# Kernel tuning notes

Hardware: AMD Instinct MI355X
Metric: run time of the kernel (lower is better)

## Reference

```python
import jax, jax.numpy as jnp
import numpy as np

B, S = 64, 32
VF, IF = 512, 256
F = VF + IF        # fused feature dim == sensory dim
U = 768            # wiring units == rnn_hidden_dim (motor_size == units)
UNFOLDS = 6        # ncps LTC default ode_unfolds
EPS = 1e-8


def setup_inputs() -> dict:
    key = jax.random.key(0)
    ks = jax.random.split(key, 24)
    d = {}
    d['fv'] = jax.random.normal(ks[0], (B, S, VF), jnp.float32)
    d['fv_alter'] = jax.random.normal(ks[1], (B, S, VF), jnp.float32)
    d['fi'] = jax.random.normal(ks[2], (B, S, IF), jnp.float32)
    d['dec'] = jax.random.normal(ks[3], (B, S, 2), jnp.float32)
    # strictly increasing timestamps so relative timespans are positive
    d['ts'] = jnp.cumsum(jax.random.uniform(ks[4], (B, S + 1), jnp.float32, 0.01, 0.1), axis=1)
    # LTC cell parameters (ncps init ranges), FullyConnected wiring -> dense masks of ones
    d['input_w'] = jnp.ones((F,), jnp.float32)
    d['input_b'] = jnp.zeros((F,), jnp.float32)
    d['sensory_mu'] = jax.random.uniform(ks[5], (F, U), jnp.float32, 0.3, 0.8)
    d['sensory_sigma'] = jax.random.uniform(ks[6], (F, U), jnp.float32, 3.0, 8.0)
    d['sensory_w'] = jax.random.uniform(ks[7], (F, U), jnp.float32, 0.001, 1.0)
    d['sensory_erev'] = jnp.sign(jax.random.normal(ks[8], (F, U), jnp.float32))
    d['mu'] = jax.random.uniform(ks[9], (U, U), jnp.float32, 0.3, 0.8)
    d['sigma'] = jax.random.uniform(ks[10], (U, U), jnp.float32, 3.0, 8.0)
    d['w'] = jax.random.uniform(ks[11], (U, U), jnp.float32, 0.001, 1.0)
    d['erev'] = jnp.sign(jax.random.normal(ks[12], (U, U), jnp.float32))
    d['gleak'] = jax.random.uniform(ks[13], (U,), jnp.float32, 0.001, 1.0)
    d['vleak'] = jax.random.uniform(ks[14], (U,), jnp.float32, -0.2, 0.2)
    d['cm'] = jax.random.uniform(ks[15], (U,), jnp.float32, 0.4, 0.6)
    d['output_w'] = jnp.ones((U,), jnp.float32)
    d['output_b'] = jnp.zeros((U,), jnp.float32)
    d['W1'] = jax.random.normal(ks[16], (U, 128), jnp.float32) / np.sqrt(U)
    d['b1'] = jnp.zeros((128,), jnp.float32)
    d['W2'] = jax.random.normal(ks[17], (128, 6), jnp.float32) / np.sqrt(128.0)
    d['b2'] = jnp.zeros((6,), jnp.float32)
    return d


def _ltc(fused, rel_ts, input_w, input_b, sensory_mu, sensory_sigma, sensory_w,
         sensory_erev, mu, sigma, w, erev, gleak, vleak, cm, output_w, output_b):
    b = fused.shape[0]
    h0 = jnp.zeros((b, U), fused.dtype)

    def step(v, xs):
        inp, elapsed = xs  # (B,F), (B,)
        x = inp * input_w + input_b
        # sensory synapse activations: (B, F, U)
        s_act = sensory_w * jax.nn.sigmoid(sensory_sigma * (x[:, :, None] - sensory_mu))
        w_num_s = jnp.einsum('bfu,fu->bu', s_act, sensory_erev)
        w_den_s = jnp.sum(s_act, axis=1)
        cm_t = cm / (elapsed[:, None] / UNFOLDS)  # (B,U)

        def unfold(vv, _):
            act = w * jax.nn.sigmoid(sigma * (vv[:, :, None] - mu))  # (B,U,U)
            num = jnp.einsum('buv,uv->bv', act, erev) + w_num_s
            den = jnp.sum(act, axis=1) + w_den_s
            vv = (cm_t * vv + gleak * vleak + num) / (cm_t + gleak + den + EPS)
            return vv, None

        v, _ = jax.lax.scan(unfold, v, None, length=UNFOLDS)
        out = v * output_w + output_b  # motor_size == units
        return v, out

    _, outs = jax.lax.scan(step, h0, (jnp.swapaxes(fused, 0, 1), rel_ts.T))
    return jnp.swapaxes(outs, 0, 1), h0  # (B,S,U)


def reference(fv, fv_alter, fi, dec, ts, input_w, input_b, sensory_mu, sensory_sigma,
              sensory_w, sensory_erev, mu, sigma, w, erev, gleak, vleak, cm,
              output_w, output_b, W1, b1, W2, b2):
    fused = jnp.concatenate([fv, fi], axis=-1)  # FusionModule 'cat'
    rel_ts = ts[:, 1:] - ts[:, :-1]
    h_seq, h0 = _ltc(fused, rel_ts, input_w, input_b, sensory_mu, sensory_sigma,
                     sensory_w, sensory_erev, mu, sigma, w, erev, gleak, vleak, cm,
                     output_w, output_b)
    x = (h_seq - h0[:, None, :]) @ W1 + b1
    x = jnp.where(x > 0, x, 0.1 * x)  # LeakyReLU(0.1)
    pose = x @ W2 + b2
    return pose[:, None], h_seq  # (B,1,S,6), (B,S,U)
```

## Files before the change

kernel.cpp:

```cpp
#include <hip/hip_runtime.h>

#define Bq 64
#define Sq 32
#define VFq 512
#define IFq 256
#define Fq 768
#define Uq 768
#define UNFq 6
#define L2E 1.44269504088896340736f
typedef unsigned long long ull;

template <int CTRL>
__device__ __forceinline__ float dpp_add(float x) {
  int t = __builtin_amdgcn_update_dpp(0, __builtin_bit_cast(int, x), CTRL, 0xF, 0xF, true);
  return x + __builtin_bit_cast(float, t);
}
__device__ __forceinline__ float swz_add4(float x) {
  int t = __builtin_amdgcn_ds_swizzle(__builtin_bit_cast(int, x), 0x101F);
  return x + __builtin_bit_cast(float, t);
}

__global__ __launch_bounds__(256) void k_prep(
    const float* __restrict__ smu, const float* __restrict__ ssig,
    const float* __restrict__ sw,  const float* __restrict__ ser,
    const float* __restrict__ rmu, const float* __restrict__ rsig,
    const float* __restrict__ rw,  const float* __restrict__ rer,
    const float* __restrict__ ts,
    float4* __restrict__ Ps, float4* __restrict__ Pr,
    float* __restrict__ iel, unsigned* __restrict__ flags)
{
  int bid = blockIdx.x, tid = threadIdx.x;
  if (bid < 1152) {
    int set = bid / 576, tile = bid % 576;
    int tv = tile / 24, tu = tile % 24;
    const float* Amu = set ? rmu : smu;
    const float* Asg = set ? rsig : ssig;
    const float* Aw  = set ? rw  : sw;
    const float* Aer = set ? rer : ser;
    float4* P = set ? Pr : Ps;
    __shared__ float4 tl[32][33];
    int cu = tid & 31, r0 = tid >> 5;
    for (int rr = 0; rr < 32; rr += 8) {
      int v = tv*32 + r0 + rr, u = tu*32 + cu;
      int idx = v*Uq + u;
      float sg = Asg[idx], m = Amu[idx], ww = Aw[idx], er = Aer[idx];
      tl[cu][r0+rr] = make_float4(-sg*L2E, sg*m*L2E, ww, ww*er);
    }
    __syncthreads();
    for (int rr = 0; rr < 32; rr += 8) {
      int u = tu*32 + r0 + rr, v = tv*32 + (tid & 31);
      P[u*Fq + v] = tl[r0+rr][tid & 31];
    }
  } else {
    for (int i = tid; i < Bq*Sq; i += 256) {
      int b = i / Sq, t = i % Sq;
      iel[i] = (float)UNFq / (ts[b*(Sq+1)+t+1] - ts[b*(Sq+1)+t]);
    }
    for (int i = tid; i < 1024; i += 256) flags[i] = 0u;
  }
}

__global__ __launch_bounds__(768) void k_sensory(
    const float* __restrict__ fv, const float* __restrict__ fi,
    const float* __restrict__ iw, const float* __restrict__ ib,
    const float4* __restrict__ Ps,
    float* __restrict__ wns, float* __restrict__ wds)
{
  __shared__ float xs[16][Fq];
  __shared__ float scr[12][8][33];
  int tid = threadIdx.x;
  int bt_tile = blockIdx.x >> 6;
  int ut = blockIdx.x & 63;
  int u0 = ut * 12, bt0 = bt_tile * 16;
  {
    float wv = iw[tid], bv = ib[tid];
    for (int j = 0; j < 16; ++j) {
      int bt = bt0 + j, b = bt >> 5, t = bt & 31;
      float raw = (tid < VFq) ? fv[(b*Sq + t)*VFq + tid]
                              : fi[(b*Sq + t)*IFq + (tid - VFq)];
      xs[j][tid] = raw * wv + bv;
    }
  }
  __syncthreads();
  int w = tid >> 6, l = tid & 63;
  const float4* P = Ps + (u0 + w)*Fq;
  #pragma unroll
  for (int pass = 0; pass < 4; ++pass) {
    float num[4], den[4];
    #pragma unroll
    for (int q = 0; q < 4; ++q) { num[q] = 0.f; den[q] = 0.f; }
    for (int i = 0; i < 12; ++i) {
      int f = l + 64*i;
      float4 p = P[f];
      #pragma unroll
      for (int q = 0; q < 4; ++q) {
        float arg = fmaf(p.x, xs[4*pass + q][f], p.y);
        float e = __builtin_amdgcn_exp2f(arg);
        float r = __builtin_amdgcn_rcpf(1.0f + e);
        den[q] = fmaf(p.z, r, den[q]);
        num[q] = fmaf(p.w, r, num[q]);
      }
    }
    #pragma unroll
    for (int q = 0; q < 4; ++q) {
      num[q] = dpp_add<0xB1>(num[q]); den[q] = dpp_add<0xB1>(den[q]);
      num[q] = dpp_add<0x4E>(num[q]); den[q] = dpp_add<0x4E>(den[q]);
      num[q] = swz_add4(num[q]);      den[q] = swz_add4(den[q]);
    }
    if ((l & 7) == 0) {
      int rep = l >> 3;
      #pragma unroll
      for (int q = 0; q < 4; ++q) {
        scr[w][rep][4*pass + q] = num[q];
        scr[w][rep][16 + 4*pass + q] = den[q];
      }
    }
    __builtin_amdgcn_sched_barrier(0);
  }
  __syncthreads();
  if (tid < 192) {
    int u = tid >> 4, j = tid & 15;
    float nt = 0.f, dt = 0.f;
    #pragma unroll
    for (int rep = 0; rep < 8; ++rep) { nt += scr[u][rep][j]; dt += scr[u][rep][16+j]; }
    int bt = bt0 + j, b = bt >> 5, t = bt & 31;
    wns[(t*Bq + b)*Uq + (u0 + u)] = nt;
    wds[(t*Bq + b)*Uq + (u0 + u)] = dt;
  }
}

__global__ __launch_bounds__(768)
void k_recurrent(
    const float4* __restrict__ Pr,
    const float* __restrict__ wns, const float* __restrict__ wds,
    float* __restrict__ vg, const float* __restrict__ iel,
    unsigned* __restrict__ flags,
    const float* __restrict__ gleak, const float* __restrict__ vleak,
    const float* __restrict__ cm, const float* __restrict__ ow,
    const float* __restrict__ ob, float* __restrict__ hout)
{
  __shared__ float4 vvP[4][Uq];
  __shared__ float2 scr2[12][8][9];
  __shared__ float sinv[16][Sq];
  __shared__ float swn[2][96], swd[2][96];
  __shared__ float sgl[12], sglvl[12], scm[12], sow[12], sob[12];
  int tid = threadIdx.x;
  int g = blockIdx.x >> 6;
  int ut = blockIdx.x & 63;
  int u0 = ut*12, b0 = g*16;
  if (tid < 512) { int j = tid >> 5, t = tid & 31; sinv[j][t] = iel[(b0+j)*Sq + t]; }
  if (tid < 12) {
    float gl0 = gleak[u0+tid];
    sgl[tid] = gl0; sglvl[tid] = gl0 * vleak[u0+tid];
    scm[tid] = cm[u0+tid]; sow[tid] = ow[u0+tid]; sob[tid] = ob[u0+tid];
  }
  #pragma unroll
  for (int q = 0; q < 4; ++q) vvP[q][tid] = make_float4(0.f, 0.f, 0.f, 0.f);
  int w = tid >> 6, l = tid & 63;
  float4 Prg[12];
  #pragma unroll
  for (int i = 0; i < 12; ++i) Prg[i] = Pr[(u0 + w)*Uq + l + 64*i];
  __syncthreads();
  int uu8 = tid >> 3, jv = tid & 7;
  for (int t = 0; t < Sq; ++t) {
    if (tid < 96) {
      swn[0][tid] = wns[(t*Bq + b0 + jv)*Uq + u0 + uu8];
      swd[0][tid] = wds[(t*Bq + b0 + jv)*Uq + u0 + uu8];
      swn[1][tid] = wns[(t*Bq + b0 + 8 + jv)*Uq + u0 + uu8];
      swd[1][tid] = wds[(t*Bq + b0 + 8 + jv)*Uq + u0 + uu8];
    }
    for (int k = 0; k < UNFq; ++k) {
      int p = t*UNFq + k;
      #pragma unroll
      for (int h = 0; h < 2; ++h) {
        int hp = 1 - h;
        float num0[4], den0[4], num1[4], den1[4];
        #pragma unroll
        for (int q = 0; q < 4; ++q) { num0[q] = 0.f; den0[q] = 0.f; }
        #pragma unroll
        for (int i = 0; i < 12; ++i) {
          int v = l + 64*i;
          float4 pp = Prg[i];
          float4 y = vvP[2*h][v];
          float r0 = __builtin_amdgcn_rcpf(1.0f + __builtin_amdgcn_exp2f(fmaf(pp.x, y.x, pp.y)));
          float r1 = __builtin_amdgcn_rcpf(1.0f + __builtin_amdgcn_exp2f(fmaf(pp.x, y.y, pp.y)));
          float r2 = __builtin_amdgcn_rcpf(1.0f + __builtin_amdgcn_exp2f(fmaf(pp.x, y.z, pp.y)));
          float r3 = __builtin_amdgcn_rcpf(1.0f + __builtin_amdgcn_exp2f(fmaf(pp.x, y.w, pp.y)));
          den0[0] = fmaf(pp.z, r0, den0[0]); num0[0] = fmaf(pp.w, r0, num0[0]);
          den0[1] = fmaf(pp.z, r1, den0[1]); num0[1] = fmaf(pp.w, r1, num0[1]);
          den0[2] = fmaf(pp.z, r2, den0[2]); num0[2] = fmaf(pp.w, r2, num0[2]);
          den0[3] = fmaf(pp.z, r3, den0[3]); num0[3] = fmaf(pp.w, r3, num0[3]);
        }
        #pragma unroll
        for (int q = 0; q < 4; ++q) {
          num0[q] = dpp_add<0xB1>(num0[q]); den0[q] = dpp_add<0xB1>(den0[q]);
          num0[q] = dpp_add<0x4E>(num0[q]); den0[q] = dpp_add<0x4E>(den0[q]);
          num0[q] = swz_add4(num0[q]);      den0[q] = swz_add4(den0[q]);
        }
        if ((l & 7) == 0) {
          int r = l >> 3;
          #pragma unroll
          for (int q = 0; q < 4; ++q) scr2[w][r][q] = make_float2(num0[q], den0[q]);
        }
        __builtin_amdgcn_sched_barrier(0);
        ull ga0 = 0, ga1 = 0, ga2 = 0, ga3 = 0;
        bool do_g = !(p == 0 && h == 0);
        if (do_g) {
          const unsigned* f = flags + hp*256 + g*64 + l;
          unsigned tgt = (unsigned)(p + h);
          while (true) {
            unsigned vf = __hip_atomic_load(f, __ATOMIC_RELAXED, __HIP_MEMORY_SCOPE_AGENT);
            if (__ballot(vf < tgt) == 0ull) break;
            __builtin_amdgcn_s_sleep(1);
          }
          const ull* src = (const ull*)(vg + (hp*4 + g)*Uq*8) + tid*4;
          ga0 = __hip_atomic_load(src + 0, __ATOMIC_RELAXED, __HIP_MEMORY_SCOPE_AGENT);
          ga1 = __hip_atomic_load(src + 1, __ATOMIC_RELAXED, __HIP_MEMORY_SCOPE_AGENT);
          ga2 = __hip_atomic_load(src + 2, __ATOMIC_RELAXED, __HIP_MEMORY_SCOPE_AGENT);
          ga3 = __hip_atomic_load(src + 3, __ATOMIC_RELAXED, __HIP_MEMORY_SCOPE_AGENT);
        }
        __builtin_amdgcn_sched_barrier(0);
        #pragma unroll
        for (int q = 0; q < 4; ++q) { num1[q] = 0.f; den1[q] = 0.f; }
        #pragma unroll
        for (int i = 0; i < 12; ++i) {
          int v = l + 64*i;
          float4 pp = Prg[i];
          float4 y = vvP[2*h+1][v];
          float r0 = __builtin_amdgcn_rcpf(1.0f + __builtin_amdgcn_exp2f(fmaf(pp.x, y.x, pp.y)));
          float r1 = __builtin_amdgcn_rcpf(1.0f + __builtin_amdgcn_exp2f(fmaf(pp.x, y.y, pp.y)));
          float r2 = __builtin_amdgcn_rcpf(1.0f + __builtin_amdgcn_exp2f(fmaf(pp.x, y.z, pp.y)));
          float r3 = __builtin_amdgcn_rcpf(1.0f + __builtin_amdgcn_exp2f(fmaf(pp.x, y.w, pp.y)));
          den1[0] = fmaf(pp.z, r0, den1[0]); num1[0] = fmaf(pp.w, r0, num1[0]);
          den1[1] = fmaf(pp.z, r1, den1[1]); num1[1] = fmaf(pp.w, r1, num1[1]);
          den1[2] = fmaf(pp.z, r2, den1[2]); num1[2] = fmaf(pp.w, r2, num1[2]);
          den1[3] = fmaf(pp.z, r3, den1[3]); num1[3] = fmaf(pp.w, r3, num1[3]);
        }
        #pragma unroll
        for (int q = 0; q < 4; ++q) {
          num1[q] = dpp_add<0xB1>(num1[q]); den1[q] = dpp_add<0xB1>(den1[q]);
          num1[q] = dpp_add<0x4E>(num1[q]); den1[q] = dpp_add<0x4E>(den1[q]);
          num1[q] = swz_add4(num1[q]);      den1[q] = swz_add4(den1[q]);
        }
        if ((l & 7) == 0) {
          int r = l >> 3;
          #pragma unroll
          for (int q = 0; q < 4; ++q) scr2[w][r][4+q] = make_float2(num1[q], den1[q]);
        }
        if (do_g) {
          float2 t0 = __builtin_bit_cast(float2, ga0);
          float2 t1 = __builtin_bit_cast(float2, ga1);
          float2 t2 = __builtin_bit_cast(float2, ga2);
          float2 t3 = __builtin_bit_cast(float2, ga3);
          vvP[2*hp+0][tid] = make_float4(t0.x, t0.y, t1.x, t1.y);
          vvP[2*hp+1][tid] = make_float4(t2.x, t2.y, t3.x, t3.y);
        }
        __syncthreads();
        if (tid < 96) {
          float nt = swn[h][tid], dt = swd[h][tid];
          #pragma unroll
          for (int r = 0; r < 8; ++r) { float2 s = scr2[uu8][r][jv]; nt += s.x; dt += s.y; }
          int jh = h*8 + jv;
          float cmt = scm[uu8] * sinv[jh][t];
          const float* vrow = (const float*)&vvP[2*h + (jv >> 2)][u0 + uu8];
          float vold = vrow[jv & 3];
          float vnew = (cmt*vold + sglvl[uu8] + nt)
                     * __builtin_amdgcn_rcpf(cmt + sgl[uu8] + dt + 1e-8f);
          __hip_atomic_store(&vg[(h*4 + g)*Uq*8 + (u0 + uu8)*8 + jv], vnew,
                             __ATOMIC_RELAXED, __HIP_MEMORY_SCOPE_AGENT);
          if (k == UNFq-1)
            hout[((b0 + jh)*Sq + t)*Uq + u0 + uu8] = fmaf(vnew, sow[uu8], sob[uu8]);
        }
        __builtin_amdgcn_s_waitcnt(0);
        __syncthreads();
        if (tid == 0)
          __hip_atomic_store(&flags[h*256 + g*64 + ut], (unsigned)(p + 1),
                             __ATOMIC_RELAXED, __HIP_MEMORY_SCOPE_AGENT);
      }
    }
  }
}

__global__ __launch_bounds__(128) void k_head(
    const float* __restrict__ hseq, const float* __restrict__ W1,
    const float* __restrict__ b1, const float* __restrict__ W2,
    const float* __restrict__ b2, float* __restrict__ pose)
{
  __shared__ float h[Uq];
  __shared__ float x1[128];
  int bt = blockIdx.x, tid = threadIdx.x;
  for (int j = 0; j < 6; ++j) h[tid + 128*j] = hseq[bt*Uq + tid + 128*j];
  __syncthreads();
  float acc = b1[tid];
  for (int f = 0; f < Uq; ++f) acc = fmaf(h[f], W1[f*128 + tid], acc);
  x1[tid] = acc > 0.f ? acc : 0.1f*acc;
  __syncthreads();
  if (tid < 6) {
    float a2 = b2[tid];
    #pragma unroll
    for (int c = 0; c < 128; ++c) a2 = fmaf(x1[c], W2[c*6 + tid], a2);
    pose[bt*6 + tid] = a2;
  }
}

extern "C" void kernel_launch(void* const* d_in, const int* in_sizes, int n_in,
                              void* d_out, int out_size, void* d_ws, size_t ws_size,
                              hipStream_t stream) {
  const float* fv   = (const float*)d_in[0];
  const float* fi   = (const float*)d_in[2];
  const float* ts   = (const float*)d_in[4];
  const float* iw   = (const float*)d_in[5];
  const float* ibb  = (const float*)d_in[6];
  const float* smu  = (const float*)d_in[7];
  const float* ssig = (const float*)d_in[8];
  const float* sw   = (const float*)d_in[9];
  const float* ser  = (const float*)d_in[10];
  const float* rmu  = (const float*)d_in[11];
  const float* rsig = (const float*)d_in[12];
  const float* rw   = (const float*)d_in[13];
  const float* rer  = (const float*)d_in[14];
  const float* gl   = (const float*)d_in[15];
  const float* vl   = (const float*)d_in[16];
  const float* cm   = (const float*)d_in[17];
  const float* ow   = (const float*)d_in[18];
  const float* ob   = (const float*)d_in[19];
  const float* W1   = (const float*)d_in[20];
  const float* b1   = (const float*)d_in[21];
  const float* W2   = (const float*)d_in[22];
  const float* b2   = (const float*)d_in[23];

  float* pose = (float*)d_out;
  float* hseq = (float*)d_out + Bq*Sq*6;

  float* ws = (float*)d_ws;
  float4* Ps = (float4*)ws;
  float4* Pr = (float4*)(ws + 2359296);
  float* wns = ws + 4718592;
  float* wds = ws + 6291456;
  float* vg  = ws + 7864320;
  float* iel = ws + 7962624;
  unsigned* flags = (unsigned*)(ws + 7964672);

  k_prep<<<1153, 256, 0, stream>>>(smu, ssig, sw, ser, rmu, rsig, rw, rer,
                                   ts, Ps, Pr, iel, flags);
  k_sensory<<<8192, 768, 0, stream>>>(fv, fi, iw, ibb, Ps, wns, wds);
  k_recurrent<<<256, 768, 0, stream>>>(Pr, wns, wds, vg, iel, flags,
                                       gl, vl, cm, ow, ob, hseq);
  k_head<<<2048, 128, 0, stream>>>(hseq, W1, b1, W2, b2, pose);
}
```

Before: 2.425 ms.

## Finalize recurrent update per wave with swizzle reductions and packed FMAs

```diff
diff --git a/kernel.cpp b/kernel.cpp
--- a/kernel.cpp
+++ b/kernel.cpp
@@ -9,14 +9,16 @@
 #define UNFq 6
 #define L2E 1.44269504088896340736f
 typedef unsigned long long ull;
+typedef __attribute__((ext_vector_type(2))) float f2;
 
 template <int CTRL>
 __device__ __forceinline__ float dpp_add(float x) {
   int t = __builtin_amdgcn_update_dpp(0, __builtin_bit_cast(int, x), CTRL, 0xF, 0xF, true);
   return x + __builtin_bit_cast(float, t);
 }
-__device__ __forceinline__ float swz_add4(float x) {
-  int t = __builtin_amdgcn_ds_swizzle(__builtin_bit_cast(int, x), 0x101F);
+template <int OFF>
+__device__ __forceinline__ float swz_add(float x) {
+  int t = __builtin_amdgcn_ds_swizzle(__builtin_bit_cast(int, x), OFF);
   return x + __builtin_bit_cast(float, t);
 }
 
@@ -86,33 +88,31 @@
   const float4* P = Ps + (u0 + w)*Fq;
   #pragma unroll
   for (int pass = 0; pass < 4; ++pass) {
-    float num[4], den[4];
+    f2 acc[4];
     #pragma unroll
-    for (int q = 0; q < 4; ++q) { num[q] = 0.f; den[q] = 0.f; }
+    for (int q = 0; q < 4; ++q) acc[q] = (f2){0.f, 0.f};
     for (int i = 0; i < 12; ++i) {
       int f = l + 64*i;
       float4 p = P[f];
+      f2 pwz = (f2){p.w, p.z};
       #pragma unroll
       for (int q = 0; q < 4; ++q) {
         float arg = fmaf(p.x, xs[4*pass + q][f], p.y);
         float e = __builtin_amdgcn_exp2f(arg);
         float r = __builtin_amdgcn_rcpf(1.0f + e);
-        den[q] = fmaf(p.z, r, den[q]);
-        num[q] = fmaf(p.w, r, num[q]);
+        acc[q] = __builtin_elementwise_fma(pwz, (f2){r, r}, acc[q]);
       }
     }
     #pragma unroll
     for (int q = 0; q < 4; ++q) {
-      num[q] = dpp_add<0xB1>(num[q]); den[q] = dpp_add<0xB1>(den[q]);
-      num[q] = dpp_add<0x4E>(num[q]); den[q] = dpp_add<0x4E>(den[q]);
-      num[q] = swz_add4(num[q]);      den[q] = swz_add4(den[q]);
-    }
-    if ((l & 7) == 0) {
-      int rep = l >> 3;
-      #pragma unroll
-      for (int q = 0; q < 4; ++q) {
-        scr[w][rep][4*pass + q] = num[q];
-        scr[w][rep][16 + 4*pass + q] = den[q];
+      float num = acc[q].x, den = acc[q].y;
+      num = dpp_add<0xB1>(num); den = dpp_add<0xB1>(den);
+      num = dpp_add<0x4E>(num); den = dpp_add<0x4E>(den);
+      num = swz_add<0x101F>(num); den = swz_add<0x101F>(den);
+      if ((l & 7) == 0) {
+        int rep = l >> 3;
+        scr[w][rep][4*pass + q] = num;
+        scr[w][rep][16 + 4*pass + q] = den;
       }
     }
     __builtin_amdgcn_sched_barrier(0);
@@ -142,65 +142,61 @@
   __shared__ float4 vvP[4][Uq];
   __shared__ float2 scr2[12][8][9];
   __shared__ float sinv[16][Sq];
-  __shared__ float swn[2][96], swd[2][96];
-  __shared__ float sgl[12], sglvl[12], scm[12], sow[12], sob[12];
   int tid = threadIdx.x;
   int g = blockIdx.x >> 6;
   int ut = blockIdx.x & 63;
   int u0 = ut*12, b0 = g*16;
   if (tid < 512) { int j = tid >> 5, t = tid & 31; sinv[j][t] = iel[(b0+j)*Sq + t]; }
-  if (tid < 12) {
-    float gl0 = gleak[u0+tid];
-    sgl[tid] = gl0; sglvl[tid] = gl0 * vleak[u0+tid];
-    scm[tid] = cm[u0+tid]; sow[tid] = ow[u0+tid]; sob[tid] = ob[u0+tid];
-  }
   #pragma unroll
   for (int q = 0; q < 4; ++q) vvP[q][tid] = make_float4(0.f, 0.f, 0.f, 0.f);
   int w = tid >> 6, l = tid & 63;
+  float my_gl   = gleak[u0 + w];
+  float my_glvl = my_gl * vleak[u0 + w];
+  float my_cm   = cm[u0 + w];
+  float my_ow   = ow[u0 + w];
+  float my_ob   = ob[u0 + w];
   float4 Prg[12];
   #pragma unroll
   for (int i = 0; i < 12; ++i) Prg[i] = Pr[(u0 + w)*Uq + l + 64*i];
   __syncthreads();
-  int uu8 = tid >> 3, jv = tid & 7;
+  int jl = l & 7;
   for (int t = 0; t < Sq; ++t) {
-    if (tid < 96) {
-      swn[0][tid] = wns[(t*Bq + b0 + jv)*Uq + u0 + uu8];
-      swd[0][tid] = wds[(t*Bq + b0 + jv)*Uq + u0 + uu8];
-      swn[1][tid] = wns[(t*Bq + b0 + 8 + jv)*Uq + u0 + uu8];
-      swd[1][tid] = wds[(t*Bq + b0 + 8 + jv)*Uq + u0 + uu8];
-    }
+    float wn0 = wns[(t*Bq + b0 + jl)*Uq + u0 + w];
+    float wd0 = wds[(t*Bq + b0 + jl)*Uq + u0 + w];
+    float wn1 = wns[(t*Bq + b0 + 8 + jl)*Uq + u0 + w];
+    float wd1 = wds[(t*Bq + b0 + 8 + jl)*Uq + u0 + w];
     for (int k = 0; k < UNFq; ++k) {
       int p = t*UNFq + k;
       #pragma unroll
       for (int h = 0; h < 2; ++h) {
         int hp = 1 - h;
-        float num0[4], den0[4], num1[4], den1[4];
-        #pragma unroll
-        for (int q = 0; q < 4; ++q) { num0[q] = 0.f; den0[q] = 0.f; }
-        #pragma unroll
-        for (int i = 0; i < 12; ++i) {
-          int v = l + 64*i;
-          float4 pp = Prg[i];
-          float4 y = vvP[2*h][v];
-          float r0 = __builtin_amdgcn_rcpf(1.0f + __builtin_amdgcn_exp2f(fmaf(pp.x, y.x, pp.y)));
-          float r1 = __builtin_amdgcn_rcpf(1.0f + __builtin_amdgcn_exp2f(fmaf(pp.x, y.y, pp.y)));
-          float r2 = __builtin_amdgcn_rcpf(1.0f + __builtin_amdgcn_exp2f(fmaf(pp.x, y.z, pp.y)));
-          float r3 = __builtin_amdgcn_rcpf(1.0f + __builtin_amdgcn_exp2f(fmaf(pp.x, y.w, pp.y)));
-          den0[0] = fmaf(pp.z, r0, den0[0]); num0[0] = fmaf(pp.w, r0, num0[0]);
-          den0[1] = fmaf(pp.z, r1, den0[1]); num0[1] = fmaf(pp.w, r1, num0[1]);
-          den0[2] = fmaf(pp.z, r2, den0[2]); num0[2] = fmaf(pp.w, r2, num0[2]);
-          den0[3] = fmaf(pp.z, r3, den0[3]); num0[3] = fmaf(pp.w, r3, num0[3]);
-        }
-        #pragma unroll
-        for (int q = 0; q < 4; ++q) {
-          num0[q] = dpp_add<0xB1>(num0[q]); den0[q] = dpp_add<0xB1>(den0[q]);
-          num0[q] = dpp_add<0x4E>(num0[q]); den0[q] = dpp_add<0x4E>(den0[q]);
-          num0[q] = swz_add4(num0[q]);      den0[q] = swz_add4(den0[q]);
-        }
-        if ((l & 7) == 0) {
-          int r = l >> 3;
-          #pragma unroll
-          for (int q = 0; q < 4; ++q) scr2[w][r][q] = make_float2(num0[q], den0[q]);
+        {
+          f2 acc[4];
+          #pragma unroll
+          for (int q = 0; q < 4; ++q) acc[q] = (f2){0.f, 0.f};
+          #pragma unroll
+          for (int i = 0; i < 12; ++i) {
+            int v = l + 64*i;
+            float4 pp = Prg[i];
+            f2 pwz = (f2){pp.w, pp.z};
+            float4 y = vvP[2*h][v];
+            float r0 = __builtin_amdgcn_rcpf(1.0f + __builtin_amdgcn_exp2f(fmaf(pp.x, y.x, pp.y)));
+            float r1 = __builtin_amdgcn_rcpf(1.0f + __builtin_amdgcn_exp2f(fmaf(pp.x, y.y, pp.y)));
+            float r2 = __builtin_amdgcn_rcpf(1.0f + __builtin_amdgcn_exp2f(fmaf(pp.x, y.z, pp.y)));
+            float r3 = __builtin_amdgcn_rcpf(1.0f + __builtin_amdgcn_exp2f(fmaf(pp.x, y.w, pp.y)));
+            acc[0] = __builtin_elementwise_fma(pwz, (f2){r0, r0}, acc[0]);
+            acc[1] = __builtin_elementwise_fma(pwz, (f2){r1, r1}, acc[1]);
+            acc[2] = __builtin_elementwise_fma(pwz, (f2){r2, r2}, acc[2]);
+            acc[3] = __builtin_elementwise_fma(pwz, (f2){r3, r3}, acc[3]);
+          }
+          #pragma unroll
+          for (int q = 0; q < 4; ++q) {
+            float num = acc[q].x, den = acc[q].y;
+            num = dpp_add<0xB1>(num); den = dpp_add<0xB1>(den);
+            num = dpp_add<0x4E>(num); den = dpp_add<0x4E>(den);
+            num = swz_add<0x101F>(num); den = swz_add<0x101F>(den);
+            if ((l & 7) == 0) scr2[w][l >> 3][q] = make_float2(num, den);
+          }
         }
         __builtin_amdgcn_sched_barrier(0);
         ull ga0 = 0, ga1 = 0, ga2 = 0, ga3 = 0;
@@ -220,32 +216,33 @@
           ga3 = __hip_atomic_load(src + 3, __ATOMIC_RELAXED, __HIP_MEMORY_SCOPE_AGENT);
         }
         __builtin_amdgcn_sched_barrier(0);
-        #pragma unroll
-        for (int q = 0; q < 4; ++q) { num1[q] = 0.f; den1[q] = 0.f; }
-        #pragma unroll
-        for (int i = 0; i < 12; ++i) {
-          int v = l + 64*i;
-          float4 pp = Prg[i];
-          float4 y = vvP[2*h+1][v];
-          float r0 = __builtin_amdgcn_rcpf(1.0f + __builtin_amdgcn_exp2f(fmaf(pp.x, y.x, pp.y)));
-          float r1 = __builtin_amdgcn_rcpf(1.0f + __builtin_amdgcn_exp2f(fmaf(pp.x, y.y, pp.y)));
-          float r2 = __builtin_amdgcn_rcpf(1.0f + __builtin_amdgcn_exp2f(fmaf(pp.x, y.z, pp.y)));
-          float r3 = __builtin_amdgcn_rcpf(1.0f + __builtin_amdgcn_exp2f(fmaf(pp.x, y.w, pp.y)));
-          den1[0] = fmaf(pp.z, r0, den1[0]); num1[0] = fmaf(pp.w, r0, num1[0]);
-          den1[1] = fmaf(pp.z, r1, den1[1]); num1[1] = fmaf(pp.w, r1, num1[1]);
-          den1[2] = fmaf(pp.z, r2, den1[2]); num1[2] = fmaf(pp.w, r2, num1[2]);
-          den1[3] = fmaf(pp.z, r3, den1[3]); num1[3] = fmaf(pp.w, r3, num1[3]);
-        }
-        #pragma unroll
-        for (int q = 0; q < 4; ++q) {
-          num1[q] = dpp_add<0xB1>(num1[q]); den1[q] = dpp_add<0xB1>(den1[q]);
-          num1[q] = dpp_add<0x4E>(num1[q]); den1[q] = dpp_add<0x4E>(den1[q]);
-          num1[q] = swz_add4(num1[q]);      den1[q] = swz_add4(den1[q]);
-        }
-        if ((l & 7) == 0) {
-          int r = l >> 3;
-          #pragma unroll
-          for (int q = 0; q < 4; ++q) scr2[w][r][4+q] = make_float2(num1[q], den1[q]);
+        {
+          f2 acc[4];
+          #pragma unroll
+          for (int q = 0; q < 4; ++q) acc[q] = (f2){0.f, 0.f};
+          #pragma unroll
+          for (int i = 0; i < 12; ++i) {
+            int v = l + 64*i;
+            float4 pp = Prg[i];
+            f2 pwz = (f2){pp.w, pp.z};
+            float4 y = vvP[2*h+1][v];
+            float r0 = __builtin_amdgcn_rcpf(1.0f + __builtin_amdgcn_exp2f(fmaf(pp.x, y.x, pp.y)));
+            float r1 = __builtin_amdgcn_rcpf(1.0f + __builtin_amdgcn_exp2f(fmaf(pp.x, y.y, pp.y)));
+            float r2 = __builtin_amdgcn_rcpf(1.0f + __builtin_amdgcn_exp2f(fmaf(pp.x, y.z, pp.y)));
+            float r3 = __builtin_amdgcn_rcpf(1.0f + __builtin_amdgcn_exp2f(fmaf(pp.x, y.w, pp.y)));
+            acc[0] = __builtin_elementwise_fma(pwz, (f2){r0, r0}, acc[0]);
+            acc[1] = __builtin_elementwise_fma(pwz, (f2){r1, r1}, acc[1]);
+            acc[2] = __builtin_elementwise_fma(pwz, (f2){r2, r2}, acc[2]);
+            acc[3] = __builtin_elementwise_fma(pwz, (f2){r3, r3}, acc[3]);
+          }
+          #pragma unroll
+          for (int q = 0; q < 4; ++q) {
+            float num = acc[q].x, den = acc[q].y;
+            num = dpp_add<0xB1>(num); den = dpp_add<0xB1>(den);
+            num = dpp_add<0x4E>(num); den = dpp_add<0x4E>(den);
+            num = swz_add<0x101F>(num); den = swz_add<0x101F>(den);
+            if ((l & 7) == 0) scr2[w][l >> 3][4 + q] = make_float2(num, den);
+          }
         }
         if (do_g) {
           float2 t0 = __builtin_bit_cast(float2, ga0);
@@ -255,21 +252,25 @@
           vvP[2*hp+0][tid] = make_float4(t0.x, t0.y, t1.x, t1.y);
           vvP[2*hp+1][tid] = make_float4(t2.x, t2.y, t3.x, t3.y);
         }
-        __syncthreads();
-        if (tid < 96) {
-          float nt = swn[h][tid], dt = swd[h][tid];
-          #pragma unroll
-          for (int r = 0; r < 8; ++r) { float2 s = scr2[uu8][r][jv]; nt += s.x; dt += s.y; }
-          int jh = h*8 + jv;
-          float cmt = scm[uu8] * sinv[jh][t];
-          const float* vrow = (const float*)&vvP[2*h + (jv >> 2)][u0 + uu8];
-          float vold = vrow[jv & 3];
-          float vnew = (cmt*vold + sglvl[uu8] + nt)
-                     * __builtin_amdgcn_rcpf(cmt + sgl[uu8] + dt + 1e-8f);
-          __hip_atomic_store(&vg[(h*4 + g)*Uq*8 + (u0 + uu8)*8 + jv], vnew,
-                             __ATOMIC_RELAXED, __HIP_MEMORY_SCOPE_AGENT);
-          if (k == UNFq-1)
-            hout[((b0 + jh)*Sq + t)*Uq + u0 + uu8] = fmaf(vnew, sow[uu8], sob[uu8]);
+        {
+          float2 me = scr2[w][l >> 3][jl];
+          float nn = me.x, dd = me.y;
+          nn = swz_add<0x201F>(nn); dd = swz_add<0x201F>(dd);
+          nn = swz_add<0x401F>(nn); dd = swz_add<0x401F>(dd);
+          nn += __shfl_xor(nn, 32, 64);      dd += __shfl_xor(dd, 32, 64);
+          if (l < 8) {
+            int jh = h*8 + jl;
+            float nt = nn + (h ? wn1 : wn0);
+            float dt = dd + (h ? wd1 : wd0);
+            float cmt = my_cm * sinv[jh][t];
+            float vold = ((const float*)&vvP[2*h + (jl >> 2)][u0 + w])[jl & 3];
+            float vnew = (cmt*vold + my_glvl + nt)
+                       * __builtin_amdgcn_rcpf(cmt + my_gl + dt + 1e-8f);
+            __hip_atomic_store(&vg[(h*4 + g)*Uq*8 + (u0 + w)*8 + jl], vnew,
+                               __ATOMIC_RELAXED, __HIP_MEMORY_SCOPE_AGENT);
+            if (k == UNFq-1)
+              hout[((b0 + jh)*Sq + t)*Uq + u0 + w] = fmaf(vnew, my_ow, my_ob);
+          }
         }
         __builtin_amdgcn_s_waitcnt(0);
         __syncthreads();
```

Measured after the change: 2.485 ms. 1.02x slower.
